# Kernel optimization log

Hardware: AMD Instinct MI355X
Metric: run time of the kernel (lower is better)

The kernel has to match this reference:

```python
import jax, jax.numpy as jnp
import numpy as np

B, T = 512, 200          # batch (trials), time bins
N = 10000                # n_neurons
SI, DI = 100, 68         # static / dynamic input sizes
HS, HD = 256, 128        # hidden_dim_static / hidden_dim_dynamic
K = 1                    # output_size
D = 2 * HD + HS          # 512, routed-GEMM contraction dim


def setup_inputs() -> dict:
    key = jax.random.key(0)
    ks = jax.random.split(key, 19)
    g = lambda i, shape, s=0.05: (jax.random.normal(ks[i], shape, jnp.float32) * s)
    return dict(
        x_static=g(0, (B, SI), 1.0),
        x_dynamic=g(1, (B, T, DI), 1.0),
        neuron_order=jax.random.randint(ks[2], (B,), 0, N),
        w_s1=g(3, (HS, SI)), b_s1=g(4, (HS,)),
        w_s2=g(5, (HS, HS)), b_s2=g(6, (HS,)),
        w_dyn=g(7, (HD, DI)), b_dyn=g(8, (HD,)),
        w_ih_f=g(9, (HD, HD)), w_hh_f=g(10, (HD, HD)),
        b_ih_f=g(11, (HD,)), b_hh_f=g(12, (HD,)),
        w_ih_b=g(13, (HD, HD)), w_hh_b=g(14, (HD, HD)),
        b_ih_b=g(15, (HD,)), b_hh_b=g(16, (HD,)),
        neuron_weights=g(17, (N, D, K)),
        neuron_bias=g(18, (N, 1, K)),
    )


def _rnn_dir(x, w_ih, w_hh, b_ih, b_hh, reverse):
    # x: [B,T,H] -> outputs [B,T,H]; torch nn.RNN with nonlinearity='relu'
    xw = jnp.einsum('bth,oh->bto', x, w_ih) + b_ih + b_hh  # precompute input proj
    h0 = jnp.zeros((x.shape[0], w_hh.shape[0]), x.dtype)

    def step(h, xt):
        h = jax.nn.relu(xt + h @ w_hh.T)
        return h, h

    _, ys = jax.lax.scan(step, h0, jnp.swapaxes(xw, 0, 1), reverse=reverse)
    return jnp.swapaxes(ys, 0, 1)


def reference(x_static, x_dynamic, neuron_order,
              w_s1, b_s1, w_s2, b_s2, w_dyn, b_dyn,
              w_ih_f, w_hh_f, b_ih_f, b_hh_f,
              w_ih_b, w_hh_b, b_ih_b, b_hh_b,
              neuron_weights, neuron_bias):
    # static branch (dropout in eval mode -> identity)
    s = jax.nn.relu(x_static @ w_s1.T + b_s1)
    s = jax.nn.relu(s @ w_s2.T + b_s2)                      # [B,HS]
    # dynamic branch
    d = jax.nn.relu(jnp.einsum('bti,oi->bto', x_dynamic, w_dyn) + b_dyn)  # [B,T,HD]
    fwd = _rnn_dir(d, w_ih_f, w_hh_f, b_ih_f, b_hh_f, reverse=False)
    bwd = _rnn_dir(d, w_ih_b, w_hh_b, b_ih_b, b_hh_b, reverse=True)
    d = jax.nn.relu(jnp.concatenate([fwd, bwd], axis=-1))   # [B,T,2*HD]
    # tile static over time and concat
    s_t = jnp.broadcast_to(s[:, None, :], (s.shape[0], d.shape[1], s.shape[1]))
    final_input = jnp.concatenate([s_t, d], axis=-1)        # [B,T,D]
    # per-sample neuron weight gather + routed batched matmul + bias + ReLU
    Wn = neuron_weights[neuron_order]                       # [B,D,K]
    bn = neuron_bias[neuron_order]                          # [B,1,K]
    out = jnp.einsum('btd,bdk->btk', final_input, Wn) + bn  # [B,T,K]
    return jax.nn.relu(jnp.squeeze(out, -1))                # [B,T] (K=1)
```

## Files before the change

kernel.cpp:

```cpp
#include <hip/hip_runtime.h>
#include <cstdint>

constexpr int B = 512, T = 200, SI = 100, DI = 68, HS = 256, HD = 128, D = 512;
constexpr int BT = B * T;

typedef __attribute__((ext_vector_type(8))) short short8;
typedef __attribute__((ext_vector_type(4))) float floatx4;
typedef _Float16 half8 __attribute__((ext_vector_type(8)));
typedef _Float16 half2t __attribute__((ext_vector_type(2)));
typedef unsigned int uint2v __attribute__((ext_vector_type(2)));
typedef unsigned int uint4v __attribute__((ext_vector_type(4)));

#define DEV __device__ __forceinline__

DEV unsigned short f2bf(float f) {
    unsigned int x = __builtin_bit_cast(unsigned int, f);
    x += 0x7fffu + ((x >> 16) & 1u);
    return (unsigned short)(x >> 16);
}
DEV unsigned int pkbf(float a, float b) {
    return (unsigned int)f2bf(a) | ((unsigned int)f2bf(b) << 16);
}
DEV unsigned short f2h(float f) {
    return __builtin_bit_cast(unsigned short, (_Float16)f);
}
DEV half2t u2h2(unsigned int u) { return __builtin_bit_cast(half2t, u); }
DEV unsigned int pkh(float a, float b) {
    return __builtin_bit_cast(unsigned int, __builtin_amdgcn_cvt_pkrtz(a, b));
}
#if __has_builtin(__builtin_amdgcn_permlane32_swap) && __has_builtin(__builtin_amdgcn_permlane16_swap)
DEV void pl32swap(unsigned int& a, unsigned int& b) {
    uint2v r = __builtin_amdgcn_permlane32_swap(a, b, false, false);
    a = r[0]; b = r[1];
}
DEV void pl16swap(unsigned int& a, unsigned int& b) {
    uint2v r = __builtin_amdgcn_permlane16_swap(a, b, false, false);
    a = r[0]; b = r[1];
}
#else
DEV void pl32swap(unsigned int& a, unsigned int& b) {
    unsigned int na, nb;
    asm("v_mov_b32 %0, %2\n\t"
        "v_mov_b32 %1, %3\n\t"
        "v_permlane32_swap_b32 %0, %1"
        : "=&v"(na), "=&v"(nb) : "v"(a), "v"(b));
    a = na; b = nb;
}
DEV void pl16swap(unsigned int& a, unsigned int& b) {
    unsigned int na, nb;
    asm("v_mov_b32 %0, %2\n\t"
        "v_mov_b32 %1, %3\n\t"
        "v_permlane16_swap_b32 %0, %1"
        : "=&v"(na), "=&v"(nb) : "v"(a), "v"(b));
    a = na; b = nb;
}
#endif

__global__ __launch_bounds__(256) void k_prep(
    const float* __restrict__ wdyn,
    const float* __restrict__ wihf, const float* __restrict__ wihb,
    const float* __restrict__ whhf, const float* __restrict__ whhb,
    const float* __restrict__ bihf, const float* __restrict__ bhhf,
    const float* __restrict__ bihb, const float* __restrict__ bhhb,
    unsigned short* __restrict__ wdyn_bf, unsigned short* __restrict__ wih_bf,
    unsigned short* __restrict__ whh_h, float* __restrict__ bsum)
{
    int gid = blockIdx.x * 256 + threadIdx.x, gs = gridDim.x * 256;
    for (int i = gid; i < HD * 96; i += gs) {
        int r = i / 96, c = i - r * 96;
        wdyn_bf[i] = (c < DI) ? f2bf(wdyn[r * DI + c]) : 0;
    }
    for (int i = gid; i < 2 * HD * HD; i += gs) {
        const float* src = (i < HD * HD) ? wihf : wihb;
        wih_bf[i] = f2bf(src[i & (HD * HD - 1)]);
    }
    for (int i = gid; i < 2 * HD * HD; i += gs) {
        const float* src = (i < HD * HD) ? whhf : whhb;
        whh_h[i] = f2h(src[i & (HD * HD - 1)]);
    }
    for (int i = gid; i < 2 * HD; i += gs) {
        int z = i >> 7, n = i & (HD - 1);
        bsum[i] = z ? (bihb[n] + bhhb[n]) : (bihf[n] + bhhf[n]);
    }
}

__global__ __launch_bounds__(256) void k_static(
    const float* __restrict__ xs_g, const float* __restrict__ w1,
    const float* __restrict__ b1, const float* __restrict__ w2,
    const float* __restrict__ b2, const int* __restrict__ norder,
    const float* __restrict__ nw, const float* __restrict__ nb,
    float* __restrict__ statd)
{
    __shared__ __align__(16) float xs[SI];
    __shared__ __align__(16) float s1[HS];
    __shared__ __align__(16) float red[256];
    int b = blockIdx.x, t = threadIdx.x;
    if (t < SI) xs[t] = xs_g[b * SI + t];
    __syncthreads();
    float a = b1[t];
    const float4* w = (const float4*)(w1 + t * SI);
    const float4* xp4 = (const float4*)xs;
    #pragma unroll
    for (int i = 0; i < SI / 4; ++i) {
        float4 ww = w[i]; float4 xx = xp4[i];
        a += xx.x * ww.x + xx.y * ww.y + xx.z * ww.z + xx.w * ww.w;
    }
    s1[t] = fmaxf(a, 0.f);
    __syncthreads();
    float a2 = b2[t];
    const float4* w2p = (const float4*)(w2 + t * HS);
    const float4* s1p = (const float4*)s1;
    #pragma unroll 8
    for (int i = 0; i < HS / 4; ++i) {
        float4 ww = w2p[i]; float4 s = s1p[i];
        a2 += s.x * ww.x + s.y * ww.y + s.z * ww.z + s.w * ww.w;
    }
    float sv = fmaxf(a2, 0.f);
    int n = norder[b];
    red[t] = sv * nw[(size_t)n * D + t];
    __syncthreads();
    for (int s = 128; s > 0; s >>= 1) {
        if (t < s) red[t] += red[t + s];
        __syncthreads();
    }
    if (t == 0) statd[b] = red[0] + nb[n];
}

__global__ __launch_bounds__(256) void k_dxw(
    const float* __restrict__ xd,
    const unsigned short* __restrict__ wdyn_bf, const float* __restrict__ bdyn,
    const unsigned short* __restrict__ wih_bf, const float* __restrict__ bsum,
    unsigned short* __restrict__ xw)
{
    __shared__ __align__(16) unsigned short xb[64][104];
    __shared__ __align__(16) unsigned short dl[64][136];
    int tid = threadIdx.x;
    int R0 = blockIdx.x * 64;
    for (int i = tid; i < 64 * 104 / 8; i += 256)
        ((uint4v*)xb)[i] = uint4v{0u, 0u, 0u, 0u};
    __syncthreads();
    for (int i = tid; i < 64 * 17; i += 256) {
        int r = i / 17, c = i - r * 17;
        float4 v = *(const float4*)(xd + (size_t)(R0 + r) * DI + c * 4);
        uint2 pk;
        pk.x = pkbf(v.x, v.y);
        pk.y = pkbf(v.z, v.w);
        *(uint2*)&xb[r][c * 4] = pk;
    }
    __syncthreads();

    int lane = tid & 63, w = tid >> 6;
    int ln = lane & 15, q = lane >> 4;

    short8 xf[3];
    #pragma unroll
    for (int c = 0; c < 3; ++c)
        xf[c] = *(const short8*)&xb[w * 16 + ln][c * 32 + q * 8];
    #pragma unroll
    for (int j = 0; j < 8; ++j) {
        floatx4 a = {0.f, 0.f, 0.f, 0.f};
        #pragma unroll
        for (int c = 0; c < 3; ++c) {
            short8 wf = *(const short8*)(wdyn_bf + (size_t)(j * 16 + ln) * 96 + c * 32 + q * 8);
            a = __builtin_amdgcn_mfma_f32_16x16x32_bf16(wf, xf[c], a, 0, 0, 0);
        }
        float4 bd4 = *(const float4*)(bdyn + j * 16 + q * 4);
        uint2 pk;
        pk.x = pkbf(fmaxf(a[0] + bd4.x, 0.f), fmaxf(a[1] + bd4.y, 0.f));
        pk.y = pkbf(fmaxf(a[2] + bd4.z, 0.f), fmaxf(a[3] + bd4.w, 0.f));
        *(uint2*)&dl[w * 16 + ln][j * 16 + q * 4] = pk;
    }
    __syncthreads();

    short8 df[4];
    #pragma unroll
    for (int c = 0; c < 4; ++c)
        df[c] = *(const short8*)&dl[w * 16 + ln][c * 32 + q * 8];
    #pragma unroll
    for (int z = 0; z < 2; ++z) {
        const unsigned short* wih = wih_bf + (size_t)z * HD * HD;
        unsigned short* outp = xw + (size_t)z * BT * HD;
        int row = R0 + w * 16 + ln;
        #pragma unroll
        for (int j = 0; j < 8; ++j) {
            floatx4 a = {0.f, 0.f, 0.f, 0.f};
            #pragma unroll
            for (int c = 0; c < 4; ++c) {
                short8 wf = *(const short8*)(wih + (size_t)(j * 16 + ln) * HD + c * 32 + q * 8);
                a = __builtin_amdgcn_mfma_f32_16x16x32_bf16(wf, df[c], a, 0, 0, 0);
            }
            float4 b4 = *(const float4*)(bsum + z * HD + j * 16 + q * 4);
            uint2 hp;
            hp.x = (unsigned int)f2h(a[0] + b4.x) | ((unsigned int)f2h(a[1] + b4.y) << 16);
            hp.y = (unsigned int)f2h(a[2] + b4.z) | ((unsigned int)f2h(a[3] + b4.w) << 16);
            *(uint2*)(outp + (size_t)row * HD + j * 16 + q * 4) = hp;
        }
    }
}

__global__ __launch_bounds__(512, 1) void k_scan(
    const unsigned short* __restrict__ xw, const unsigned short* __restrict__ whh_h,
    const int* __restrict__ norder, const float* __restrict__ nw,
    float* __restrict__ accf, float* __restrict__ accb)
{
    __shared__ __align__(16) uint4v hxch[2][4][64];

    int tid = threadIdx.x, w = tid >> 6, l = tid & 63, ln = l & 15, q = l >> 4;
    int dir = blockIdx.x >> 5, b0 = (blockIdx.x & 31) * 16;
    const unsigned short* whh = whh_h + (size_t)dir * HD * HD;
    float* acc = (dir ? accb : accf) + (size_t)w * BT;
    int segoff = dir ? (HS + HD) : HS;

    half8 wfr[4];
    #pragma unroll
    for (int c = 0; c < 4; ++c)
        wfr[c] = *(const half8*)(whh + (size_t)(w * 16 + ln) * HD + c * 32 + q * 8);

    int nrow = norder[b0 + ln];
    float4 wnl = *(const float4*)(nw + (size_t)nrow * D + segoff + w * 16 + q * 4);

    half8 hf[4];
    uint4v zz = {0u, 0u, 0u, 0u};
    #pragma unroll
    for (int c = 0; c < 4; ++c) hf[c] = __builtin_bit_cast(half8, zz);

    const unsigned short* xp = xw + ((size_t)dir * BT + (size_t)(b0 + ln) * T) * HD
                               + w * 16 + q * 4;
    float* accp = acc + (size_t)(b0 + ln) * T;
    int tstart = dir ? (T - 1) : 0, dt = dir ? -1 : 1;

    int wc = w >> 1;
    int qp = 2 * (w & 1) + (q >> 1);
    int boff = (q & 1) * 8;

    uint2 x0, x1, x2, x3;
    auto ld = [&](uint2& xb, int idx) {
        xb = *(const uint2*)(xp + (size_t)(tstart + dt * idx) * HD);
    };
    auto step = [&](uint2& xc, int idx) {
        int t = tstart + dt * idx;
        int par = idx & 1;
        half2t lo = u2h2(xc.x), hi = u2h2(xc.y);
        floatx4 a0 = {(float)lo[0], (float)lo[1], (float)hi[0], (float)hi[1]};
        floatx4 a1 = {0.f, 0.f, 0.f, 0.f};
        a0 = __builtin_amdgcn_mfma_f32_16x16x32_f16(wfr[0], hf[0], a0, 0, 0, 0);
        a1 = __builtin_amdgcn_mfma_f32_16x16x32_f16(wfr[1], hf[1], a1, 0, 0, 0);
        a0 = __builtin_amdgcn_mfma_f32_16x16x32_f16(wfr[2], hf[2], a0, 0, 0, 0);
        a1 = __builtin_amdgcn_mfma_f32_16x16x32_f16(wfr[3], hf[3], a1, 0, 0, 0);
        floatx4 a = a0 + a1;
        float r0 = fmaxf(a[0], 0.f), r1 = fmaxf(a[1], 0.f);
        float r2 = fmaxf(a[2], 0.f), r3 = fmaxf(a[3], 0.f);
        uint2 hp;
        hp.x = pkh(r0, r1);
        hp.y = pkh(r2, r3);
        *(uint2*)((char*)&hxch[par][wc][qp * 16 + ln] + boff) = hp;
        float p = r0 * wnl.x + r1 * wnl.y + r2 * wnl.z + r3 * wnl.w;
        unsigned int pa = __builtin_bit_cast(unsigned int, p), pb = pa;
        pl32swap(pa, pb);
        float ps = __builtin_bit_cast(float, pa) + __builtin_bit_cast(float, pb);
        unsigned int pc = __builtin_bit_cast(unsigned int, ps), pd = pc;
        pl16swap(pc, pd);
        float ptot = __builtin_bit_cast(float, pc) + __builtin_bit_cast(float, pd);
        if (l < 16) accp[t] = ptot;
        asm volatile("s_waitcnt lgkmcnt(0)" ::: "memory");
        __builtin_amdgcn_sched_barrier(0);
        __builtin_amdgcn_s_barrier();
        __builtin_amdgcn_sched_barrier(0);
        #pragma unroll
        for (int c = 0; c < 4; ++c)
            hf[c] = __builtin_bit_cast(half8, hxch[par][c][l]);
    };

    ld(x0, 0); ld(x1, 1); ld(x2, 2); ld(x3, 3);
    for (int c = 0; c < T / 4 - 1; ++c) {
        int i0 = c * 4;
        step(x0, i0);     ld(x0, i0 + 4);
        step(x1, i0 + 1); ld(x1, i0 + 5);
        step(x2, i0 + 2); ld(x2, i0 + 6);
        step(x3, i0 + 3); ld(x3, i0 + 7);
    }
    step(x0, T - 4);
    step(x1, T - 3);
    step(x2, T - 2);
    step(x3, T - 1);
}

__global__ __launch_bounds__(256) void k_final(
    const float* __restrict__ statd, const float* __restrict__ accf,
    const float* __restrict__ accb, float* __restrict__ out)
{
    int idx = blockIdx.x * 256 + threadIdx.x;
    if (idx < BT) {
        int b = idx / T;
        float s = statd[b];
        #pragma unroll
        for (int w = 0; w < 8; ++w)
            s += accf[(size_t)w * BT + idx] + accb[(size_t)w * BT + idx];
        out[idx] = fmaxf(s, 0.f);
    }
}

extern "C" void kernel_launch(void* const* d_in, const int* in_sizes, int n_in,
                              void* d_out, int out_size, void* d_ws, size_t ws_size,
                              hipStream_t stream)
{
    const float* x_static  = (const float*)d_in[0];
    const float* x_dynamic = (const float*)d_in[1];
    const int*   norder    = (const int*)d_in[2];
    const float* w_s1   = (const float*)d_in[3];
    const float* b_s1   = (const float*)d_in[4];
    const float* w_s2   = (const float*)d_in[5];
    const float* b_s2   = (const float*)d_in[6];
    const float* w_dyn  = (const float*)d_in[7];
    const float* b_dyn  = (const float*)d_in[8];
    const float* w_ih_f = (const float*)d_in[9];
    const float* w_hh_f = (const float*)d_in[10];
    const float* b_ih_f = (const float*)d_in[11];
    const float* b_hh_f = (const float*)d_in[12];
    const float* w_ih_b = (const float*)d_in[13];
    const float* w_hh_b = (const float*)d_in[14];
    const float* b_ih_b = (const float*)d_in[15];
    const float* b_hh_b = (const float*)d_in[16];
    const float* nw     = (const float*)d_in[17];
    const float* nb     = (const float*)d_in[18];
    float* out = (float*)d_out;

    char* ws = (char*)d_ws;
    float* statd = (float*)ws;
    float* accf  = (float*)(ws + 2048);
    float* accb  = (float*)(ws + 2048 + (size_t)8 * BT * 4);
    unsigned short* xw = (unsigned short*)(ws + 2048 + (size_t)16 * BT * 4);
    size_t xw_bytes = (size_t)2 * BT * HD * 2;
    unsigned short* wdyn_bf = (unsigned short*)(ws + 2048 + (size_t)16 * BT * 4 + xw_bytes);
    unsigned short* wih_bf  = wdyn_bf + HD * 96;
    unsigned short* whh_h   = wih_bf + 2 * HD * HD;
    float* bsum = (float*)(whh_h + 2 * HD * HD);

    hipLaunchKernelGGL(k_prep, dim3(64), dim3(256), 0, stream,
                       w_dyn, w_ih_f, w_ih_b, w_hh_f, w_hh_b,
                       b_ih_f, b_hh_f, b_ih_b, b_hh_b,
                       wdyn_bf, wih_bf, whh_h, bsum);
    hipLaunchKernelGGL(k_static, dim3(B), dim3(256), 0, stream,
                       x_static, w_s1, b_s1, w_s2, b_s2, norder, nw, nb, statd);
    hipLaunchKernelGGL(k_dxw, dim3(BT / 64), dim3(256), 0, stream,
                       x_dynamic, wdyn_bf, b_dyn, wih_bf, bsum, xw);
    hipLaunchKernelGGL(k_scan, dim3(64), dim3(512), 0, stream,
                       xw, whh_h, norder, nw, accf, accb);
    hipLaunchKernelGGL(k_final, dim3((BT + 255) / 256), dim3(256), 0, stream,
                       statd, accf, accb, out);
}
```

Baseline: 278.2 us.

## Make k_dxw persistent with register-resident weights and prefetch next tile

Turns the input-projection kernel into a persistent kernel with 256 blocks that loop over row tiles. The bf16 w_dyn and both w_ih matrices are loaded once into registers per block, replacing the per-tile global weight reloads. The next tile's input is staged into shared memory while the current tile's second GEMM runs. This needs many registers (about 88 short8 fragments per thread), so there is a spill risk, and occupancy falls to one block per CU.

After: 244.5 us. 1.14x faster.

```diff
diff --git a/kernel.cpp b/kernel.cpp
--- a/kernel.cpp
+++ b/kernel.cpp
@@ -3,6 +3,7 @@
 
 constexpr int B = 512, T = 200, SI = 100, DI = 68, HS = 256, HD = 128, D = 512;
 constexpr int BT = B * T;
+constexpr int NT = BT / 64;
 
 typedef __attribute__((ext_vector_type(8))) short short8;
 typedef __attribute__((ext_vector_type(4))) float floatx4;
@@ -126,7 +127,7 @@
     if (t == 0) statd[b] = red[0] + nb[n];
 }
 
-__global__ __launch_bounds__(256) void k_dxw(
+__global__ __launch_bounds__(256, 1) void k_dxw(
     const float* __restrict__ xd,
     const unsigned short* __restrict__ wdyn_bf, const float* __restrict__ bdyn,
     const unsigned short* __restrict__ wih_bf, const float* __restrict__ bsum,
@@ -135,66 +136,87 @@
     __shared__ __align__(16) unsigned short xb[64][104];
     __shared__ __align__(16) unsigned short dl[64][136];
     int tid = threadIdx.x;
-    int R0 = blockIdx.x * 64;
+    int lane = tid & 63, w = tid >> 6;
+    int ln = lane & 15, q = lane >> 4;
+
+    short8 wdf[8][3];
+    #pragma unroll
+    for (int j = 0; j < 8; ++j)
+        #pragma unroll
+        for (int c = 0; c < 3; ++c)
+            wdf[j][c] = *(const short8*)(wdyn_bf + (size_t)(j * 16 + ln) * 96 + c * 32 + q * 8);
+    short8 wif[2][8][4];
+    #pragma unroll
+    for (int z = 0; z < 2; ++z)
+        #pragma unroll
+        for (int j = 0; j < 8; ++j)
+            #pragma unroll
+            for (int c = 0; c < 4; ++c)
+                wif[z][j][c] = *(const short8*)(wih_bf + (size_t)z * HD * HD +
+                    (size_t)(j * 16 + ln) * HD + c * 32 + q * 8);
+
     for (int i = tid; i < 64 * 104 / 8; i += 256)
         ((uint4v*)xb)[i] = uint4v{0u, 0u, 0u, 0u};
+
+    auto stage = [&](int tile) {
+        int R0 = tile * 64;
+        for (int i = tid; i < 64 * 17; i += 256) {
+            int r = i / 17, c = i - r * 17;
+            float4 v = *(const float4*)(xd + (size_t)(R0 + r) * DI + c * 4);
+            uint2 pk;
+            pk.x = pkbf(v.x, v.y);
+            pk.y = pkbf(v.z, v.w);
+            *(uint2*)&xb[r][c * 4] = pk;
+        }
+    };
+
+    stage(blockIdx.x);
     __syncthreads();
-    for (int i = tid; i < 64 * 17; i += 256) {
-        int r = i / 17, c = i - r * 17;
-        float4 v = *(const float4*)(xd + (size_t)(R0 + r) * DI + c * 4);
-        uint2 pk;
-        pk.x = pkbf(v.x, v.y);
-        pk.y = pkbf(v.z, v.w);
-        *(uint2*)&xb[r][c * 4] = pk;
-    }
-    __syncthreads();
-
-    int lane = tid & 63, w = tid >> 6;
-    int ln = lane & 15, q = lane >> 4;
-
-    short8 xf[3];
-    #pragma unroll
-    for (int c = 0; c < 3; ++c)
-        xf[c] = *(const short8*)&xb[w * 16 + ln][c * 32 + q * 8];
-    #pragma unroll
-    for (int j = 0; j < 8; ++j) {
-        floatx4 a = {0.f, 0.f, 0.f, 0.f};
-        #pragma unroll
-        for (int c = 0; c < 3; ++c) {
-            short8 wf = *(const short8*)(wdyn_bf + (size_t)(j * 16 + ln) * 96 + c * 32 + q * 8);
-            a = __builtin_amdgcn_mfma_f32_16x16x32_bf16(wf, xf[c], a, 0, 0, 0);
-        }
-        float4 bd4 = *(const float4*)(bdyn + j * 16 + q * 4);
-        uint2 pk;
-        pk.x = pkbf(fmaxf(a[0] + bd4.x, 0.f), fmaxf(a[1] + bd4.y, 0.f));
-        pk.y = pkbf(fmaxf(a[2] + bd4.z, 0.f), fmaxf(a[3] + bd4.w, 0.f));
-        *(uint2*)&dl[w * 16 + ln][j * 16 + q * 4] = pk;
-    }
-    __syncthreads();
-
-    short8 df[4];
-    #pragma unroll
-    for (int c = 0; c < 4; ++c)
-        df[c] = *(const short8*)&dl[w * 16 + ln][c * 32 + q * 8];
-    #pragma unroll
-    for (int z = 0; z < 2; ++z) {
-        const unsigned short* wih = wih_bf + (size_t)z * HD * HD;
-        unsigned short* outp = xw + (size_t)z * BT * HD;
-        int row = R0 + w * 16 + ln;
+
+    for (int tile = blockIdx.x; tile < NT; tile += gridDim.x) {
+        int R0 = tile * 64;
+        short8 xf[3];
+        #pragma unroll
+        for (int c = 0; c < 3; ++c)
+            xf[c] = *(const short8*)&xb[w * 16 + ln][c * 32 + q * 8];
         #pragma unroll
         for (int j = 0; j < 8; ++j) {
             floatx4 a = {0.f, 0.f, 0.f, 0.f};
             #pragma unroll
-            for (int c = 0; c < 4; ++c) {
-                short8 wf = *(const short8*)(wih + (size_t)(j * 16 + ln) * HD + c * 32 + q * 8);
-                a = __builtin_amdgcn_mfma_f32_16x16x32_bf16(wf, df[c], a, 0, 0, 0);
+            for (int c = 0; c < 3; ++c)
+                a = __builtin_amdgcn_mfma_f32_16x16x32_bf16(wdf[j][c], xf[c], a, 0, 0, 0);
+            float4 bd4 = *(const float4*)(bdyn + j * 16 + q * 4);
+            uint2 pk;
+            pk.x = pkbf(fmaxf(a[0] + bd4.x, 0.f), fmaxf(a[1] + bd4.y, 0.f));
+            pk.y = pkbf(fmaxf(a[2] + bd4.z, 0.f), fmaxf(a[3] + bd4.w, 0.f));
+            *(uint2*)&dl[w * 16 + ln][j * 16 + q * 4] = pk;
+        }
+        __syncthreads();
+
+        int nxt = tile + gridDim.x;
+        if (nxt < NT) stage(nxt);
+        short8 df[4];
+        #pragma unroll
+        for (int c = 0; c < 4; ++c)
+            df[c] = *(const short8*)&dl[w * 16 + ln][c * 32 + q * 8];
+        int row = R0 + w * 16 + ln;
+        #pragma unroll
+        for (int z = 0; z < 2; ++z) {
+            unsigned short* outp = xw + (size_t)z * BT * HD;
+            #pragma unroll
+            for (int j = 0; j < 8; ++j) {
+                floatx4 a = {0.f, 0.f, 0.f, 0.f};
+                #pragma unroll
+                for (int c = 0; c < 4; ++c)
+                    a = __builtin_amdgcn_mfma_f32_16x16x32_bf16(wif[z][j][c], df[c], a, 0, 0, 0);
+                float4 b4 = *(const float4*)(bsum + z * HD + j * 16 + q * 4);
+                uint2 hp;
+                hp.x = (unsigned int)f2h(a[0] + b4.x) | ((unsigned int)f2h(a[1] + b4.y) << 16);
+                hp.y = (unsigned int)f2h(a[2] + b4.z) | ((unsigned int)f2h(a[3] + b4.w) << 16);
+                *(uint2*)(outp + (size_t)row * HD + j * 16 + q * 4) = hp;
             }
-            float4 b4 = *(const float4*)(bsum + z * HD + j * 16 + q * 4);
-            uint2 hp;
-            hp.x = (unsigned int)f2h(a[0] + b4.x) | ((unsigned int)f2h(a[1] + b4.y) << 16);
-            hp.y = (unsigned int)f2h(a[2] + b4.z) | ((unsigned int)f2h(a[3] + b4.w) << 16);
-            *(uint2*)(outp + (size_t)row * HD + j * 16 + q * 4) = hp;
         }
+        __syncthreads();
     }
 }
 
@@ -342,7 +364,7 @@
                        wdyn_bf, wih_bf, whh_h, bsum);
     hipLaunchKernelGGL(k_static, dim3(B), dim3(256), 0, stream,
                        x_static, w_s1, b_s1, w_s2, b_s2, norder, nw, nb, statd);
-    hipLaunchKernelGGL(k_dxw, dim3(BT / 64), dim3(256), 0, stream,
+    hipLaunchKernelGGL(k_dxw, dim3(256), dim3(256), 0, stream,
                        x_dynamic, wdyn_bf, b_dyn, wih_bf, bsum, xw);
     hipLaunchKernelGGL(k_scan, dim3(64), dim3(512), 0, stream,
                        xw, whh_h, norder, nw, accf, accb);
```
